# Kernel tuning notes

Measured on AMD Instinct MI355X. Metric: run time of the kernel, lower is better.

Reference implementation:

```python
import jax, jax.numpy as jnp
import numpy as np

D_MODEL = 1024
D_INNER = 4096
K = 127
B, L = 2, 4096

def setup_inputs() -> dict:
    key = jax.random.key(0)
    k1, k2, k3, k4, k5 = jax.random.split(key, 5)
    x = jax.random.normal(k1, (B, L, D_MODEL), dtype=jnp.float32)
    # in_proj: Linear(d, 2*m) -> weight [2m, d] (torch convention)
    w_in = jax.random.normal(k2, (2 * D_INNER, D_MODEL), dtype=jnp.float32) * (1.0 / np.sqrt(D_MODEL))
    # depthwise conv weight: [m, 1, k] in torch; store as [m, k]
    w_dw = jax.random.normal(k3, (D_INNER, K), dtype=jnp.float32) * (1.0 / np.sqrt(K))
    b_dw = jax.random.normal(k4, (D_INNER,), dtype=jnp.float32) * 0.01
    # out_proj: Linear(m, d) -> weight [d, m]
    w_out = jax.random.normal(k5, (D_MODEL, D_INNER), dtype=jnp.float32) * (1.0 / np.sqrt(D_INNER))
    return {"x": x, "w_in": w_in, "w_dw": w_dw, "b_dw": b_dw, "w_out": w_out}

def _causal_dwconv(v, w_dw, b_dw):
    # v: [B, L, m]; causal depthwise conv with kernel K
    # pad K-1 on the left only (equivalent to torch pad=K-1 then [..., :L])
    v_bcl = jnp.transpose(v, (0, 2, 1))  # [B, m, L]
    out = jax.lax.conv_general_dilated(
        v_bcl,
        w_dw[:, None, :],  # [m, 1, K]
        window_strides=(1,),
        padding=[(K - 1, 0)],
        feature_group_count=D_INNER,
        dimension_numbers=("NCH", "OIH", "NCH"),
    )
    out = out + b_dw[None, :, None]
    return jnp.transpose(out, (0, 2, 1))  # [B, L, m]

def reference(x, w_in, w_dw, b_dw, w_out):
    vg = jnp.einsum("bld,ed->ble", x, w_in)  # [B, L, 2m]
    v, g = jnp.split(vg, 2, axis=-1)
    v = _causal_dwconv(v, w_dw, b_dw)
    y = jax.nn.silu(v) * jax.nn.silu(g)
    return jnp.einsum("blm,dm->bld", y, w_out)
```

## Files before the change

### kernel.cpp

```cpp
#include <hip/hip_runtime.h>
#include <hip/hip_bf16.h>
#include <cstdint>
#include <cstddef>

typedef __fp16 f16_t;
typedef __attribute__((ext_vector_type(8))) __fp16 f16x8;
typedef __attribute__((ext_vector_type(4))) __fp16 f16x4;
typedef __attribute__((ext_vector_type(2))) __fp16 h2_t;
typedef __attribute__((ext_vector_type(4))) float floatx4;

__device__ __forceinline__ void async_copy_16B(const void* g, void* l) {
  __builtin_amdgcn_global_load_lds(
      (const __attribute__((address_space(1))) void*)g,
      (__attribute__((address_space(3))) void*)l, 16, 0, 0);
}

__global__ __launch_bounds__(256) void prep(
    const float* __restrict__ x, const float* __restrict__ w_in,
    const float* __restrict__ w_out, const float* __restrict__ w_dw,
    f16_t* __restrict__ x_h, f16_t* __restrict__ wi_h,
    f16_t* __restrict__ wo_h, h2_t* __restrict__ wp) {
  const int tid = blockIdx.x * 256 + threadIdx.x;
  if (tid < 5242880) {
    const float* src;
    f16_t* dst;
    int off;
    if (tid < 2097152) {
      src = x; dst = x_h; off = tid;
    } else if (tid < 4194304) {
      src = w_in; dst = wi_h; off = tid - 2097152;
    } else {
      src = w_out; dst = wo_h; off = tid - 4194304;
    }
    const float4 v = *(const float4*)(src + (size_t)off * 4);
    f16x4 o;
    o.x = (f16_t)v.x; o.y = (f16_t)v.y; o.z = (f16_t)v.z; o.w = (f16_t)v.w;
    *(f16x4*)(dst + (size_t)off * 4) = o;
  } else {
    const int idx = tid - 5242880;
    if (idx < 128 * 4096) {
      const int p = idx >> 12;
      const int c = idx & 4095;
      float a, b;
      if (p < 126) {
        a = w_dw[c * 127 + p]; b = w_dw[c * 127 + p + 1];
      } else if (p == 126) {
        a = w_dw[c * 127 + 126]; b = 0.f;
      } else {
        a = 0.f; b = w_dw[c * 127 + 0];
      }
      h2_t w;
      w.x = (f16_t)a; w.y = (f16_t)b;
      wp[idx] = w;
    }
  }
}

template <int BN_, typename OutT>
__global__ __launch_bounds__(256) void gemm_bt64(
    const f16_t* __restrict__ A, const f16_t* __restrict__ B,
    OutT* __restrict__ C, int M, int N, int K) {
  constexpr int BM_ = 128;
  constexpr int FI = (BN_ == 128) ? 4 : 2;
  constexpr int FJ = 4;
  constexpr int ACH = BM_ * 8;
  constexpr int CH = (BM_ + BN_) * 8;
  constexpr int CPT = CH / 256;

  __shared__ f16_t smem[(BM_ + BN_) * 64];
  f16_t* const As0 = smem;
  f16_t* const As1 = smem + BM_ * 32;
  f16_t* const Bs0 = smem + BM_ * 64;
  f16_t* const Bs1 = smem + BM_ * 64 + BN_ * 32;

  const int t = threadIdx.x;
  const int lane = t & 63;
  const int wave = t >> 6;
  const int m0 = blockIdx.y * BM_;
  const int n0 = blockIdx.x * BN_;
  const int wr = (BN_ == 128) ? (wave >> 1) * 64 : wave * 32;
  const int wc = (BN_ == 128) ? (wave & 1) * 64 : 0;
  const int fr = lane & 15;
  const int fk = (lane >> 4) * 8;

  floatx4 acc[FI][FJ] = {};

  const int kTiles = K / 64;
  for (int kt = 0; kt < kTiles; ++kt) {
    const int k0 = kt * 64;
    __syncthreads();
#pragma unroll
    for (int it = 0; it < CPT; ++it) {
      const int p = it * 256 + t;
      const f16_t* gsrc;
      if (p < BM_ * 4) {
        const int row = p >> 2, kc = (p & 3) * 8;
        gsrc = A + (size_t)(m0 + row) * K + k0 + kc;
      } else if (p < ACH) {
        const int q = p - BM_ * 4;
        const int row = q >> 2, kc = 32 + (q & 3) * 8;
        gsrc = A + (size_t)(m0 + row) * K + k0 + kc;
      } else if (p < ACH + BN_ * 4) {
        const int q = p - ACH;
        const int row = q >> 2, kc = (q & 3) * 8;
        gsrc = B + (size_t)(n0 + row) * K + k0 + kc;
      } else {
        const int q = p - ACH - BN_ * 4;
        const int row = q >> 2, kc = 32 + (q & 3) * 8;
        gsrc = B + (size_t)(n0 + row) * K + k0 + kc;
      }
      async_copy_16B(gsrc, smem + p * 8);
    }
    __syncthreads();

    f16x8 af[FI][2], bfr[FJ][2];
#pragma unroll
    for (int i = 0; i < FI; ++i) {
      const int r = (wr + i * 16 + fr) * 32 + fk;
      af[i][0] = *(const f16x8*)(As0 + r);
      af[i][1] = *(const f16x8*)(As1 + r);
    }
#pragma unroll
    for (int j = 0; j < FJ; ++j) {
      const int r = (wc + j * 16 + fr) * 32 + fk;
      bfr[j][0] = *(const f16x8*)(Bs0 + r);
      bfr[j][1] = *(const f16x8*)(Bs1 + r);
    }
#pragma unroll
    for (int h = 0; h < 2; ++h)
#pragma unroll
      for (int i = 0; i < FI; ++i)
#pragma unroll
        for (int j = 0; j < FJ; ++j)
          acc[i][j] = __builtin_amdgcn_mfma_f32_16x16x32_f16(
              af[i][h], bfr[j][h], acc[i][j], 0, 0, 0);
  }

  const int cr = (lane >> 4) * 4;
  const int cc = lane & 15;
#pragma unroll
  for (int i = 0; i < FI; ++i)
#pragma unroll
    for (int j = 0; j < FJ; ++j)
#pragma unroll
      for (int r = 0; r < 4; ++r) {
        const int row = m0 + wr + i * 16 + cr + r;
        const int col = n0 + wc + j * 16 + cc;
        C[(size_t)row * N + col] = (OutT)acc[i][j][r];
      }
}

__global__ __launch_bounds__(256) void gemm_bt_k128(
    const f16_t* __restrict__ A, const f16_t* __restrict__ B,
    float* __restrict__ C, int M, int N, int K) {
  constexpr int BM_ = 128, BN_ = 64, KP = 4;
  constexpr int NA = BM_ * 4 * KP;
  constexpr int NTOT = (BM_ + BN_) * 4 * KP;
  constexpr int CPT = NTOT / 256;

  __shared__ f16_t smem[(BM_ + BN_) * 128];
  const int t = threadIdx.x;
  const int lane = t & 63;
  const int wave = t >> 6;
  const int m0 = blockIdx.y * BM_;
  const int n0 = blockIdx.x * BN_;
  const int wr = wave * 32;
  const int fr = lane & 15;
  const int fk = (lane >> 4) * 8;

  floatx4 acc[2][4] = {};

  const int kTiles = K / 128;
  for (int kt = 0; kt < kTiles; ++kt) {
    const int k0 = kt * 128;
    __syncthreads();
#pragma unroll
    for (int it = 0; it < CPT; ++it) {
      const int p = it * 256 + t;
      const f16_t* gsrc;
      if (p < NA) {
        const int h = p >> 9;
        const int r = (p >> 2) & (BM_ - 1);
        const int kc = h * 32 + (p & 3) * 8;
        gsrc = A + (size_t)(m0 + r) * K + k0 + kc;
      } else {
        const int q = p - NA;
        const int h = q >> 8;
        const int r = (q >> 2) & (BN_ - 1);
        const int kc = h * 32 + (q & 3) * 8;
        gsrc = B + (size_t)(n0 + r) * K + k0 + kc;
      }
      async_copy_16B(gsrc, smem + p * 8);
    }
    __syncthreads();

#pragma unroll
    for (int h = 0; h < KP; ++h) {
      f16x8 af[2], bf[4];
#pragma unroll
      for (int i = 0; i < 2; ++i)
        af[i] = *(const f16x8*)(smem + h * BM_ * 32 + (wr + i * 16 + fr) * 32 + fk);
#pragma unroll
      for (int j = 0; j < 4; ++j)
        bf[j] = *(const f16x8*)(smem + NA * 8 + h * BN_ * 32 + (j * 16 + fr) * 32 + fk);
#pragma unroll
      for (int i = 0; i < 2; ++i)
#pragma unroll
        for (int j = 0; j < 4; ++j)
          acc[i][j] = __builtin_amdgcn_mfma_f32_16x16x32_f16(
              af[i], bf[j], acc[i][j], 0, 0, 0);
    }
  }

  const int cr = (lane >> 4) * 4;
  const int cc = lane & 15;
#pragma unroll
  for (int i = 0; i < 2; ++i)
#pragma unroll
    for (int j = 0; j < 4; ++j)
#pragma unroll
      for (int r = 0; r < 4; ++r) {
        const int row = m0 + wr + i * 16 + cr + r;
        const int col = n0 + j * 16 + cc;
        C[(size_t)row * N + col] = acc[i][j][r];
      }
}

#define CONV_L 128
#define CPAIRS 127

__global__ __launch_bounds__(256) void conv_gate(
    const f16_t* __restrict__ vg, const h2_t* __restrict__ wp,
    const float* __restrict__ b_dw, f16_t* __restrict__ y) {
  __shared__ uint32_t vtp[CPAIRS * 64];
  __shared__ uint32_t wpl[128 * 64];
  const int t = threadIdx.x;
  const int lane = t & 63;
  const int wave = t >> 6;
  const int c0 = blockIdx.x * 64;
  const int lt = blockIdx.y & 31;
  const int b = blockIdx.y >> 5;
  const int l0 = lt * CONV_L;

#pragma unroll
  for (int it = 0; it < 8; ++it) {
    const int q = it * 256 + t;
    async_copy_16B(wp + (size_t)(q >> 4) * 4096 + c0 + (q & 15) * 4,
                   wpl + q * 4);
  }
  for (int q = t; q < CPAIRS * 8; q += 256) {
    const int m = q >> 3;
    const int oc = (q & 7) * 8;
    const int le = l0 - 126 + 2 * m;
    uint4 a = make_uint4(0u, 0u, 0u, 0u);
    uint4 bb = make_uint4(0u, 0u, 0u, 0u);
    if (le >= 0) {
      const size_t base = (size_t)(b * 4096 + le) * 8192 + c0 + oc;
      a = *(const uint4*)(vg + base);
      bb = *(const uint4*)(vg + base + 8192);
    }
    uint32_t* dst = vtp + m * 64 + oc;
    const uint32_t aw[4] = {a.x, a.y, a.z, a.w};
    const uint32_t bw[4] = {bb.x, bb.y, bb.z, bb.w};
#pragma unroll
    for (int i = 0; i < 4; ++i) {
      dst[2 * i] = (aw[i] & 0xFFFFu) | (bw[i] << 16);
      dst[2 * i + 1] = (aw[i] >> 16) | (bw[i] & 0xFFFF0000u);
    }
  }

  const int c = c0 + lane;
  const int lb = l0 + wave * 32;
  const f16_t* gp = vg + (size_t)(b * 4096 + lb) * 8192 + 4096 + c;
  f16_t gvals[32];
#pragma unroll
  for (int i = 0; i < 32; ++i) gvals[i] = gp[(size_t)i * 8192];

  __syncthreads();

  const float bias = b_dw[c];
  float acc[32];
#pragma unroll
  for (int i = 0; i < 32; ++i) acc[i] = bias;

  const uint32_t* vbase = vtp + wave * 16 * 64 + lane;
  const uint32_t* wbase = wpl + lane;

  h2_t ring[17];
#pragma unroll
  for (int m = 0; m < 17; ++m)
    ring[m] = __builtin_bit_cast(h2_t, vbase[m * 64]);

  {
    const h2_t w0 = __builtin_bit_cast(h2_t, wbase[127 * 64]);
#pragma unroll
    for (int h = 0; h < 16; ++h)
      acc[2 * h + 1] =
          __builtin_amdgcn_fdot2(w0, ring[h], acc[2 * h + 1], false);
  }

#pragma unroll
  for (int k = 0; k < 64; ++k) {
    const h2_t we = __builtin_bit_cast(h2_t, wbase[(2 * k) * 64]);
#pragma unroll
    for (int h = 0; h < 16; ++h)
      acc[2 * h] =
          __builtin_amdgcn_fdot2(we, ring[(k + h) % 17], acc[2 * h], false);
    if (k < 63) {
      const h2_t wo = __builtin_bit_cast(h2_t, wbase[(2 * k + 1) * 64]);
#pragma unroll
      for (int h = 0; h < 16; ++h)
        acc[2 * h + 1] = __builtin_amdgcn_fdot2(wo, ring[(k + 1 + h) % 17],
                                                acc[2 * h + 1], false);
      if (k < 62)
        ring[k % 17] = __builtin_bit_cast(h2_t, vbase[(17 + k) * 64]);
    }
  }

  f16_t* yp = y + (size_t)(b * 4096 + lb) * 4096 + c;
#pragma unroll
  for (int i = 0; i < 32; ++i) {
    const float gv = (float)gvals[i];
    const float v = acc[i];
    const float sv = v / (1.f + __expf(-v));
    const float sg = gv / (1.f + __expf(-gv));
    yp[(size_t)i * 4096] = (f16_t)(sv * sg);
  }
}

extern "C" void kernel_launch(void* const* d_in, const int* in_sizes, int n_in,
                              void* d_out, int out_size, void* d_ws,
                              size_t ws_size, hipStream_t stream) {
  const float* x     = (const float*)d_in[0];
  const float* w_in  = (const float*)d_in[1];
  const float* w_dw  = (const float*)d_in[2];
  const float* b_dw  = (const float*)d_in[3];
  const float* w_out = (const float*)d_in[4];
  float* out = (float*)d_out;

  char* p = (char*)d_ws;
  f16_t* x_h  = (f16_t*)p; p += (size_t)8192 * 1024 * 2;
  f16_t* wi_h = (f16_t*)p; p += (size_t)8192 * 1024 * 2;
  f16_t* wo_h = (f16_t*)p; p += (size_t)1024 * 4096 * 2;
  h2_t*  wp   = (h2_t*)p;  p += (size_t)128 * 4096 * 4;
  f16_t* vg   = (f16_t*)p; p += (size_t)8192 * 8192 * 2;
  f16_t* y    = (f16_t*)p; p += (size_t)8192 * 4096 * 2;

  prep<<<22528, 256, 0, stream>>>(x, w_in, w_out, w_dw, x_h, wi_h, wo_h, wp);

  gemm_bt64<128, f16_t><<<dim3(64, 64), 256, 0, stream>>>(x_h, wi_h, vg,
                                                          8192, 8192, 1024);
  conv_gate<<<dim3(64, 64), 256, 0, stream>>>(vg, wp, b_dw, y);
  gemm_bt_k128<<<dim3(16, 64), 256, 0, stream>>>(y, wo_h, out,
                                                 8192, 1024, 4096);
}
```

Measured before the change: 485.4 us.

## Replace in_proj GEMM with 256x256 double-buffered swizzled-LDS pipelined kernel

Replaces the 128x128-tile in-projection GEMM with a 512-thread kernel that computes a 256x256 output tile per block. It uses XOR-swizzled LDS layouts and double-buffered async global-to-LDS loads, issuing the next tile's loads in stages interleaved with MFMA work under explicit vmcnt waits. It also adds a grouped block-index swizzle for L2 reuse and raises wave priority around the MFMA bursts. The aim is more data reuse per LDS byte and overlap of memory with compute. In exchange it needs 128KB of dynamic LDS, so occupancy drops to one block per CU, and the hand-tuned waitcnt counts are fragile.

```diff
diff --git a/kernel.cpp b/kernel.cpp
--- a/kernel.cpp
+++ b/kernel.cpp
@@ -14,6 +14,8 @@
       (const __attribute__((address_space(1))) void*)g,
       (__attribute__((address_space(3))) void*)l, 16, 0, 0);
 }
+
+#define ISSUE_FENCE asm volatile("" ::: "memory")
 
 __global__ __launch_bounds__(256) void prep(
     const float* __restrict__ x, const float* __restrict__ w_in,
@@ -56,97 +58,124 @@
   }
 }
 
-template <int BN_, typename OutT>
-__global__ __launch_bounds__(256) void gemm_bt64(
+__global__ __launch_bounds__(512, 2) void gemm256_8p(
     const f16_t* __restrict__ A, const f16_t* __restrict__ B,
-    OutT* __restrict__ C, int M, int N, int K) {
-  constexpr int BM_ = 128;
-  constexpr int FI = (BN_ == 128) ? 4 : 2;
-  constexpr int FJ = 4;
-  constexpr int ACH = BM_ * 8;
-  constexpr int CH = (BM_ + BN_) * 8;
-  constexpr int CPT = CH / 256;
-
-  __shared__ f16_t smem[(BM_ + BN_) * 64];
-  f16_t* const As0 = smem;
-  f16_t* const As1 = smem + BM_ * 32;
-  f16_t* const Bs0 = smem + BM_ * 64;
-  f16_t* const Bs1 = smem + BM_ * 64 + BN_ * 32;
-
+    f16_t* __restrict__ C, int M, int N, int K) {
+  extern __shared__ char smem[];
   const int t = threadIdx.x;
   const int lane = t & 63;
   const int wave = t >> 6;
-  const int m0 = blockIdx.y * BM_;
-  const int n0 = blockIdx.x * BN_;
-  const int wr = (BN_ == 128) ? (wave >> 1) * 64 : wave * 32;
-  const int wc = (BN_ == 128) ? (wave & 1) * 64 : 0;
+  const int wm = wave >> 2;
+  const int wn = wave & 3;
+
+  const int bid = blockIdx.x;
+  const int swz = (bid & 7) * 128 + (bid >> 3);
+  const int m0 = (swz >> 5) * 256;
+  const int n0 = (swz & 31) * 256;
+
   const int fr = lane & 15;
-  const int fk = (lane >> 4) * 8;
-
-  floatx4 acc[FI][FJ] = {};
-
+  const int ks = lane >> 4;
+
+  auto stageB = [&](int d, int k0, int half) {
+#pragma unroll
+    for (int l = 0; l < 2; ++l) {
+      const int q = l * 512 + t;
+      const int row = half * 128 + (q >> 3);
+      const int slot = q & 7;
+      const int col = (slot ^ (row & 7)) * 8;
+      async_copy_16B(B + (size_t)(n0 + row) * K + k0 + col,
+                     smem + d * 65536 + 32768 + row * 128 + slot * 16);
+    }
+  };
+  auto stageA = [&](int d, int k0, int j) {
+    const int blk = t >> 8;
+    const int row = j * 32 + blk * 128 + ((t & 255) >> 3);
+    const int slot = t & 7;
+    const int col = (slot ^ (row & 7)) * 8;
+    async_copy_16B(A + (size_t)(m0 + row) * K + k0 + col,
+                   smem + d * 65536 + row * 128 + slot * 16);
+  };
+  auto ldA = [&](int d, int R, int kslot) -> f16x8 {
+    return *(const f16x8*)(smem + d * 65536 + R * 128 +
+                           ((kslot ^ (R & 7)) << 4));
+  };
+  auto ldB = [&](int d, int R, int kslot) -> f16x8 {
+    return *(const f16x8*)(smem + d * 65536 + 32768 + R * 128 +
+                           ((kslot ^ (R & 7)) << 4));
+  };
+
+  floatx4 acc[8][4] = {};
   const int kTiles = K / 64;
-  for (int kt = 0; kt < kTiles; ++kt) {
-    const int k0 = kt * 64;
-    __syncthreads();
-#pragma unroll
-    for (int it = 0; it < CPT; ++it) {
-      const int p = it * 256 + t;
-      const f16_t* gsrc;
-      if (p < BM_ * 4) {
-        const int row = p >> 2, kc = (p & 3) * 8;
-        gsrc = A + (size_t)(m0 + row) * K + k0 + kc;
-      } else if (p < ACH) {
-        const int q = p - BM_ * 4;
-        const int row = q >> 2, kc = 32 + (q & 3) * 8;
-        gsrc = A + (size_t)(m0 + row) * K + k0 + kc;
-      } else if (p < ACH + BN_ * 4) {
-        const int q = p - ACH;
-        const int row = q >> 2, kc = (q & 3) * 8;
-        gsrc = B + (size_t)(n0 + row) * K + k0 + kc;
+
+  stageB(0, 0, 0); ISSUE_FENCE;
+  stageB(0, 0, 1); ISSUE_FENCE;
+  stageA(0, 0, 0); ISSUE_FENCE;
+  stageA(0, 0, 1); ISSUE_FENCE;
+  stageA(0, 0, 2); ISSUE_FENCE;
+  stageA(0, 0, 3); ISSUE_FENCE;
+  asm volatile("s_waitcnt vmcnt(3)" ::: "memory");
+  __builtin_amdgcn_s_barrier();
+
+  f16x8 bf[4][2];
+  for (int tt = 0; tt < kTiles; ++tt) {
+    const int d = tt & 1;
+    const int kn = (tt + 1) * 64;
+    const bool pf = (tt + 1 < kTiles);
+#pragma unroll
+    for (int q = 0; q < 4; ++q) {
+      f16x8 af[2][2];
+#pragma unroll
+      for (int kh = 0; kh < 2; ++kh) {
+#pragma unroll
+        for (int ii = 0; ii < 2; ++ii)
+          af[ii][kh] = ldA(d, wm * 128 + q * 32 + ii * 16 + fr, kh * 4 + ks);
+        if (q == 0)
+#pragma unroll
+          for (int j = 0; j < 4; ++j)
+            bf[j][kh] = ldB(d, wn * 64 + j * 16 + fr, kh * 4 + ks);
+      }
+      if (pf) {
+        if (q == 0) stageB(d ^ 1, kn, 0);
+        else if (q == 1) stageB(d ^ 1, kn, 1);
+        else if (q == 2) { stageA(d ^ 1, kn, 0); stageA(d ^ 1, kn, 1); }
+        else { stageA(d ^ 1, kn, 2); stageA(d ^ 1, kn, 3); }
+      }
+      if (pf) {
+        if (q == 0)      asm volatile("s_waitcnt vmcnt(4)" ::: "memory");
+        else if (q == 1) asm volatile("s_waitcnt vmcnt(5)" ::: "memory");
+        else if (q == 2) asm volatile("s_waitcnt vmcnt(6)" ::: "memory");
+        else             asm volatile("s_waitcnt vmcnt(3)" ::: "memory");
       } else {
-        const int q = p - ACH - BN_ * 4;
-        const int row = q >> 2, kc = 32 + (q & 3) * 8;
-        gsrc = B + (size_t)(n0 + row) * K + k0 + kc;
-      }
-      async_copy_16B(gsrc, smem + p * 8);
-    }
-    __syncthreads();
-
-    f16x8 af[FI][2], bfr[FJ][2];
-#pragma unroll
-    for (int i = 0; i < FI; ++i) {
-      const int r = (wr + i * 16 + fr) * 32 + fk;
-      af[i][0] = *(const f16x8*)(As0 + r);
-      af[i][1] = *(const f16x8*)(As1 + r);
-    }
-#pragma unroll
-    for (int j = 0; j < FJ; ++j) {
-      const int r = (wc + j * 16 + fr) * 32 + fk;
-      bfr[j][0] = *(const f16x8*)(Bs0 + r);
-      bfr[j][1] = *(const f16x8*)(Bs1 + r);
-    }
-#pragma unroll
-    for (int h = 0; h < 2; ++h)
-#pragma unroll
-      for (int i = 0; i < FI; ++i)
-#pragma unroll
-        for (int j = 0; j < FJ; ++j)
-          acc[i][j] = __builtin_amdgcn_mfma_f32_16x16x32_f16(
-              af[i][h], bfr[j][h], acc[i][j], 0, 0, 0);
+        if (q == 0)      asm volatile("s_waitcnt vmcnt(2)" ::: "memory");
+        else if (q == 1) asm volatile("s_waitcnt vmcnt(1)" ::: "memory");
+        else if (q == 2) asm volatile("s_waitcnt vmcnt(0)" ::: "memory");
+      }
+      __builtin_amdgcn_s_barrier();
+      __builtin_amdgcn_s_setprio(1);
+#pragma unroll
+      for (int kh = 0; kh < 2; ++kh)
+#pragma unroll
+        for (int ii = 0; ii < 2; ++ii)
+#pragma unroll
+          for (int j = 0; j < 4; ++j)
+            acc[q * 2 + ii][j] = __builtin_amdgcn_mfma_f32_16x16x32_f16(
+                af[ii][kh], bf[j][kh], acc[q * 2 + ii][j], 0, 0, 0);
+      __builtin_amdgcn_s_setprio(0);
+      __builtin_amdgcn_s_barrier();
+    }
   }
 
   const int cr = (lane >> 4) * 4;
   const int cc = lane & 15;
 #pragma unroll
-  for (int i = 0; i < FI; ++i)
-#pragma unroll
-    for (int j = 0; j < FJ; ++j)
+  for (int i = 0; i < 8; ++i)
+#pragma unroll
+    for (int j = 0; j < 4; ++j)
 #pragma unroll
       for (int r = 0; r < 4; ++r) {
-        const int row = m0 + wr + i * 16 + cr + r;
-        const int col = n0 + wc + j * 16 + cc;
-        C[(size_t)row * N + col] = (OutT)acc[i][j][r];
+        const int row = m0 + wm * 128 + i * 16 + cr + r;
+        const int col = n0 + wn * 64 + j * 16 + cc;
+        C[(size_t)row * N + col] = (f16_t)acc[i][j][r];
       }
 }
 
@@ -348,8 +377,10 @@
 
   prep<<<22528, 256, 0, stream>>>(x, w_in, w_out, w_dw, x_h, wi_h, wo_h, wp);
 
-  gemm_bt64<128, f16_t><<<dim3(64, 64), 256, 0, stream>>>(x_h, wi_h, vg,
-                                                          8192, 8192, 1024);
+  hipFuncSetAttribute(reinterpret_cast<const void*>(gemm256_8p),
+                      hipFuncAttributeMaxDynamicSharedMemorySize, 131072);
+  gemm256_8p<<<1024, 512, 131072, stream>>>(x_h, wi_h, vg, 8192, 8192, 1024);
+
   conv_gate<<<dim3(64, 64), 256, 0, stream>>>(vg, wp, b_dw, y);
   gemm_bt_k128<<<dim3(16, 64), 256, 0, stream>>>(y, wo_h, out,
                                                  8192, 1024, 4096);
```

Result: slower. 502.6 us (+3.6%).
